# Optimization experiments

Hardware: AMD Instinct MI355X
Metric: run time of the kernel (lower is better)

The kernel has to match this reference:

```python
import jax, jax.numpy as jnp
import numpy as np

SEP = 2            # sep_token_id
B, S, H = 8, 4096, 768
MAX_SENT = 64      # = labels.size(1) in the original
STD = 0.02         # initializer_range


def setup_inputs() -> dict:
    key = jax.random.key(0)
    ks = jax.random.split(key, 6)
    hidden = jax.random.normal(ks[0], (B, S, H), jnp.float32)
    ids = jax.random.randint(ks[1], (B, S), 5, 30000, dtype=jnp.int64)
    # plant a sep every 64 tokens -> 64 seps, 64 non-empty sentences per row
    ids = ids.at[:, 63::64].set(SEP)
    W1 = jax.random.normal(ks[2], (H, 4096), jnp.float32) * STD
    b1 = jnp.zeros((4096,), jnp.float32)
    W2 = jax.random.normal(ks[3], (4096, 256), jnp.float32) * STD
    b2 = jnp.zeros((256,), jnp.float32)
    W3 = jax.random.normal(ks[4], (256, 2), jnp.float32) * STD
    b3 = jnp.zeros((2,), jnp.float32)
    return dict(hidden=hidden, input_ids=ids, W1=W1, b1=b1, W2=W2, b2=b2, W3=W3, b3=b3)


def _pool_row(h, ids):
    # h: [S, H], ids: [S] -> per-sentence means [MAX_SENT, H]
    sep = (ids == SEP)
    sep_i = sep.astype(jnp.int32)
    # exclusive cumsum: segment id = number of seps strictly before position t
    seg = jnp.cumsum(sep_i) - sep_i
    pos = jnp.arange(S)
    first_sep = jnp.argmax(sep)
    n_sep = sep_i.sum()
    # original includes the FIRST sep in sentence 0 but excludes later seps,
    # and excludes the last token of the trailing (post-last-sep) segment
    weight = jnp.where(sep, pos == first_sep, True)
    weight = weight & ~((pos == S - 1) & (seg == n_sep) & (n_sep > 0))
    # truncate to max_sentences: overflow segments land in a dump bucket
    seg_c = jnp.minimum(seg, MAX_SENT)
    hw = jnp.where(weight[:, None], h, 0.0)
    sums = jax.ops.segment_sum(hw, seg_c, num_segments=MAX_SENT + 1)[:MAX_SENT]
    cnts = jax.ops.segment_sum(weight.astype(h.dtype), seg_c, num_segments=MAX_SENT + 1)[:MAX_SENT]
    # empty (padding) segments -> zeros, matching the original zero-padding
    return jnp.where(cnts[:, None] > 0, sums / jnp.maximum(cnts, 1.0)[:, None], 0.0)


def reference(hidden, input_ids, W1, b1, W2, b2, W3, b3):
    # [B, MAX_SENT, H] per-sentence mean representations
    sent = jax.vmap(_pool_row)(hidden, input_ids)
    # classifier head (dropout = identity in eval); GELU is exact (torch nn.GELU default)
    x = jax.nn.gelu(jnp.einsum('bmh,hf->bmf', sent, W1) + b1, approximate=False)
    x = jax.nn.gelu(jnp.einsum('bmf,fg->bmg', x, W2) + b2, approximate=False)
    logits = jnp.einsum('bmg,gc->bmc', x, W3) + b3  # [B, MAX_SENT, 2]
    return logits
```

## Files before the change

### kernel.cpp

```cpp
#include <hip/hip_runtime.h>
#include <hip/hip_bf16.h>

#define SEP_ID 2
#define S_LEN  4096
#define HID    768
#define MAXS   64

using short8  = __attribute__((ext_vector_type(8))) short;
using floatx4 = __attribute__((ext_vector_type(4))) float;

__device__ __forceinline__ float gelu_exact(float x) {
    return 0.5f * x * (1.0f + erff(x * 0.70710678118654752f));
}

__global__ __launch_bounds__(256) void stage1_kernel(const int* __restrict__ ids,
                                                     const float* __restrict__ hidden,
                                                     const float* __restrict__ W1,
                                                     const float* __restrict__ W2,
                                                     __hip_bfloat16* __restrict__ W1T,
                                                     __hip_bfloat16* __restrict__ W2T,
                                                     __hip_bfloat16* __restrict__ sentb) {
    __shared__ __align__(16) char smem[16640];
    const int blk = blockIdx.x;
    const int t = threadIdx.x;

    if (blk < 512) {
        int* sep_pos = (int*)smem;
        int* wtot    = sep_pos + 4096;
        const int sidx = blk;
        const int b = sidx >> 6, m = sidx & 63;
        const int* row = ids + (size_t)b * S_LEN;
        const int lane = t & 63, w = t >> 6;

        int local[16]; int c = 0;
        const int base = t * 16;
        #pragma unroll
        for (int q = 0; q < 4; ++q) {
            int4 v = ((const int4*)row)[t * 4 + q];
            if (v.x == SEP_ID) local[c++] = base + q * 4 + 0;
            if (v.y == SEP_ID) local[c++] = base + q * 4 + 1;
            if (v.z == SEP_ID) local[c++] = base + q * 4 + 2;
            if (v.w == SEP_ID) local[c++] = base + q * 4 + 3;
        }
        int scan = c;
        #pragma unroll
        for (int off = 1; off < 64; off <<= 1) {
            int n = __shfl_up(scan, off);
            if (lane >= off) scan += n;
        }
        if (lane == 63) wtot[w] = scan;
        __syncthreads();
        int wbase = 0;
        for (int i = 0; i < w; ++i) wbase += wtot[i];
        const int o = wbase + scan - c;
        for (int i = 0; i < c; ++i) sep_pos[o + i] = local[i];
        __syncthreads();
        const int n_sep = wtot[0] + wtot[1] + wtot[2] + wtot[3];

        int start = 0, cnt = 0;
        if (n_sep == 0) {
            if (m == 0) { start = 0; cnt = S_LEN; }
        } else if (m < n_sep) {
            if (m == 0) { start = 0; cnt = sep_pos[0] + 1; }
            else { start = sep_pos[m - 1] + 1; cnt = sep_pos[m] - sep_pos[m - 1] - 1; }
        } else if (m == n_sep) {
            start = sep_pos[n_sep - 1] + 1;
            cnt = (S_LEN - 1) - start;
            if (cnt < 0) cnt = 0;
        }

        if (t < 192) {
            const float4* bp = (const float4*)(hidden + ((size_t)b * S_LEN + start) * HID);
            float ax = 0.f, ay = 0.f, az = 0.f, aw = 0.f;
            int i = 0;
            for (; i + 8 <= cnt; i += 8) {
                float4 v[8];
                #pragma unroll
                for (int j = 0; j < 8; ++j) v[j] = bp[(size_t)(i + j) * 192 + t];
                #pragma unroll
                for (int j = 0; j < 8; ++j) { ax += v[j].x; ay += v[j].y; az += v[j].z; aw += v[j].w; }
            }
            for (; i < cnt; ++i) {
                float4 v = bp[(size_t)i * 192 + t];
                ax += v.x; ay += v.y; az += v.z; aw += v.w;
            }
            const float inv = (cnt > 0) ? 1.0f / (float)cnt : 0.0f;
            __hip_bfloat16* o2 = sentb + (size_t)sidx * HID + t * 4;
            o2[0] = __float2bfloat16(ax * inv);
            o2[1] = __float2bfloat16(ay * inv);
            o2[2] = __float2bfloat16(az * inv);
            o2[3] = __float2bfloat16(aw * inv);
        }
    } else {
        float* tile = (float*)smem;
        const int id0 = blk - 512;
        const float* in; __hip_bfloat16* outw; int K, N, n0, k0;
        if (id0 < 3072) { in = W1; outw = W1T; K = 768;  N = 4096;
                          n0 = (id0 & 127) * 32; k0 = (id0 >> 7) * 32; }
        else { const int id = id0 - 3072;
               in = W2; outw = W2T; K = 4096; N = 256;
               n0 = (id & 7) * 32; k0 = (id >> 3) * 32; }
        const int c = t & 31;
        const int r = t >> 5;
        #pragma unroll
        for (int i = 0; i < 32; i += 8)
            tile[(r + i) * 33 + c] = in[(size_t)(k0 + r + i) * N + n0 + c];
        __syncthreads();
        #pragma unroll
        for (int i = 0; i < 32; i += 8)
            outw[(size_t)(n0 + r + i) * K + k0 + c] = __float2bfloat16(tile[c * 33 + r + i]);
    }
}

__global__ __launch_bounds__(256) void gemm1_kernel(const __hip_bfloat16* __restrict__ A,
                                                    const __hip_bfloat16* __restrict__ BT,
                                                    const float* __restrict__ bias,
                                                    __hip_bfloat16* __restrict__ out) {
    const int n0 = blockIdx.x * 64;
    const int m0 = blockIdx.y * 64;
    const int t = threadIdx.x;
    const int w = t >> 6, l = t & 63;
    const int wm = (w >> 1) * 32;
    const int wn = (w & 1) * 32;

    __shared__ __hip_bfloat16 Al[64][72];
    __shared__ __hip_bfloat16 Bl[64][72];

    floatx4 acc[2][2] = {};

    const int r  = t >> 2;
    const int ch = (t & 3) * 16;
    const __hip_bfloat16* Ag = A  + (size_t)(m0 + r) * 768 + ch;
    const __hip_bfloat16* Bg = BT + (size_t)(n0 + r) * 768 + ch;

    const int lr = l & 15;
    const int kq = (l >> 4) * 8;

    for (int k0 = 0; k0 < 768; k0 += 64) {
        short8 av0 = *(const short8*)(Ag + k0);
        short8 av1 = *(const short8*)(Ag + k0 + 8);
        short8 bv0 = *(const short8*)(Bg + k0);
        short8 bv1 = *(const short8*)(Bg + k0 + 8);
        __syncthreads();
        *(short8*)(&Al[r][ch])     = av0;
        *(short8*)(&Al[r][ch + 8]) = av1;
        *(short8*)(&Bl[r][ch])     = bv0;
        *(short8*)(&Bl[r][ch + 8]) = bv1;
        __syncthreads();

        #pragma unroll
        for (int ks = 0; ks < 64; ks += 32) {
            short8 a0 = *(const short8*)(&Al[wm + lr][ks + kq]);
            short8 a1 = *(const short8*)(&Al[wm + 16 + lr][ks + kq]);
            short8 b0 = *(const short8*)(&Bl[wn + lr][ks + kq]);
            short8 b1 = *(const short8*)(&Bl[wn + 16 + lr][ks + kq]);
            acc[0][0] = __builtin_amdgcn_mfma_f32_16x16x32_bf16(a0, b0, acc[0][0], 0, 0, 0);
            acc[0][1] = __builtin_amdgcn_mfma_f32_16x16x32_bf16(a0, b1, acc[0][1], 0, 0, 0);
            acc[1][0] = __builtin_amdgcn_mfma_f32_16x16x32_bf16(a1, b0, acc[1][0], 0, 0, 0);
            acc[1][1] = __builtin_amdgcn_mfma_f32_16x16x32_bf16(a1, b1, acc[1][1], 0, 0, 0);
        }
    }

    #pragma unroll
    for (int i = 0; i < 2; ++i) {
        #pragma unroll
        for (int j = 0; j < 2; ++j) {
            const int col  = n0 + wn + j * 16 + lr;
            const int rowb = m0 + wm + i * 16 + (l >> 4) * 4;
            const float bv = bias[col];
            #pragma unroll
            for (int rg = 0; rg < 4; ++rg) {
                float x = acc[i][j][rg] + bv;
                out[(size_t)(rowb + rg) * 4096 + col] = __float2bfloat16(gelu_exact(x));
            }
        }
    }
}

__global__ __launch_bounds__(256) void gemm2_kernel(const __hip_bfloat16* __restrict__ A,
                                                    const __hip_bfloat16* __restrict__ BT,
                                                    float* __restrict__ part) {
    const int n0 = blockIdx.x * 64;
    const int m0 = blockIdx.y * 64;
    const int s  = blockIdx.z;
    const int kb = s * 256;
    const int t = threadIdx.x;
    const int w = t >> 6, l = t & 63;
    const int wm = (w >> 1) * 32;
    const int wn = (w & 1) * 32;

    __shared__ __hip_bfloat16 Al[64][72];
    __shared__ __hip_bfloat16 Bl[64][72];

    floatx4 acc[2][2] = {};

    const int r  = t >> 2;
    const int ch = (t & 3) * 16;
    const __hip_bfloat16* Ag = A  + (size_t)(m0 + r) * 4096 + kb + ch;
    const __hip_bfloat16* Bg = BT + (size_t)(n0 + r) * 4096 + kb + ch;

    const int lr = l & 15;
    const int kq = (l >> 4) * 8;

    for (int k0 = 0; k0 < 256; k0 += 64) {
        short8 av0 = *(const short8*)(Ag + k0);
        short8 av1 = *(const short8*)(Ag + k0 + 8);
        short8 bv0 = *(const short8*)(Bg + k0);
        short8 bv1 = *(const short8*)(Bg + k0 + 8);
        __syncthreads();
        *(short8*)(&Al[r][ch])     = av0;
        *(short8*)(&Al[r][ch + 8]) = av1;
        *(short8*)(&Bl[r][ch])     = bv0;
        *(short8*)(&Bl[r][ch + 8]) = bv1;
        __syncthreads();

        #pragma unroll
        for (int ks = 0; ks < 64; ks += 32) {
            short8 a0 = *(const short8*)(&Al[wm + lr][ks + kq]);
            short8 a1 = *(const short8*)(&Al[wm + 16 + lr][ks + kq]);
            short8 b0 = *(const short8*)(&Bl[wn + lr][ks + kq]);
            short8 b1 = *(const short8*)(&Bl[wn + 16 + lr][ks + kq]);
            acc[0][0] = __builtin_amdgcn_mfma_f32_16x16x32_bf16(a0, b0, acc[0][0], 0, 0, 0);
            acc[0][1] = __builtin_amdgcn_mfma_f32_16x16x32_bf16(a0, b1, acc[0][1], 0, 0, 0);
            acc[1][0] = __builtin_amdgcn_mfma_f32_16x16x32_bf16(a1, b0, acc[1][0], 0, 0, 0);
            acc[1][1] = __builtin_amdgcn_mfma_f32_16x16x32_bf16(a1, b1, acc[1][1], 0, 0, 0);
        }
    }

    float* po = part + (size_t)s * 512 * 256;
    #pragma unroll
    for (int i = 0; i < 2; ++i) {
        #pragma unroll
        for (int j = 0; j < 2; ++j) {
            const int col  = n0 + wn + j * 16 + lr;
            const int rowb = m0 + wm + i * 16 + (l >> 4) * 4;
            #pragma unroll
            for (int rg = 0; rg < 4; ++rg)
                po[(size_t)(rowb + rg) * 256 + col] = acc[i][j][rg];
        }
    }
}

__global__ __launch_bounds__(256) void rh_kernel(const float* __restrict__ part,
                                                 const float* __restrict__ b2,
                                                 const float* __restrict__ W3,
                                                 const float* __restrict__ b3,
                                                 float* __restrict__ out) {
    const int row = blockIdx.x;
    const int c = threadIdx.x;
    const int w = c >> 6, l = c & 63;

    float s = 0.f;
    #pragma unroll
    for (int k = 0; k < 16; ++k)
        s += part[((size_t)k * 512 + row) * 256 + c];
    const float x = gelu_exact(s + b2[c]);
    float y0 = x * W3[c * 2 + 0];
    float y1 = x * W3[c * 2 + 1];
    #pragma unroll
    for (int off = 32; off; off >>= 1) {
        y0 += __shfl_down(y0, off);
        y1 += __shfl_down(y1, off);
    }
    __shared__ float r0[4], r1[4];
    if (l == 0) { r0[w] = y0; r1[w] = y1; }
    __syncthreads();
    if (c == 0) out[row * 2 + 0] = r0[0] + r0[1] + r0[2] + r0[3] + b3[0];
    if (c == 1) out[row * 2 + 1] = r1[0] + r1[1] + r1[2] + r1[3] + b3[1];
}

extern "C" void kernel_launch(void* const* d_in, const int* in_sizes, int n_in,
                              void* d_out, int out_size, void* d_ws, size_t ws_size,
                              hipStream_t stream) {
    const float* hidden = (const float*)d_in[0];
    const int*   ids    = (const int*)d_in[1];
    const float* W1     = (const float*)d_in[2];
    const float* b1     = (const float*)d_in[3];
    const float* W2     = (const float*)d_in[4];
    const float* b2     = (const float*)d_in[5];
    const float* W3     = (const float*)d_in[6];
    const float* b3     = (const float*)d_in[7];
    float* out = (float*)d_out;

    char* ws = (char*)d_ws;
    __hip_bfloat16* sentb  = (__hip_bfloat16*)(ws + 0);
    __hip_bfloat16* W1T    = (__hip_bfloat16*)(ws + 786432);
    __hip_bfloat16* W2T    = (__hip_bfloat16*)(ws + 7077888);
    __hip_bfloat16* x1     = (__hip_bfloat16*)(ws + 9175040);
    float* part            = (float*)(ws + 13369344);

    stage1_kernel<<<4608, 256, 0, stream>>>(ids, hidden, W1, W2, W1T, W2T, sentb);
    gemm1_kernel<<<dim3(64, 8), 256, 0, stream>>>(sentb, W1T, b1, x1);
    gemm2_kernel<<<dim3(4, 8, 16), 256, 0, stream>>>(x1, W2T, part);
    rh_kernel<<<512, 256, 0, stream>>>(part, b2, W3, b3, out);
}
```

Measured before the change: 195.4 us.

## Double GEMM k-tile depth, halve split-K, stage epilogue through LDS

Both GEMMs now load 128-wide k-tiles instead of 64-wide, halving the number of barrier pairs per k-loop. GEMM2's split-K drops from 16 to 8 slices, so the reduction kernel reads fewer partial buffers. GEMM1's epilogue writes GELU results to shared memory and then stores coalesced 16-byte rows, and the pooled sentence output is written as one packed 8-byte store. The cost is more LDS per block and only 256 blocks for GEMM2, which lowers parallelism on a device with many CUs.

```diff
diff --git a/kernel.cpp b/kernel.cpp
--- a/kernel.cpp
+++ b/kernel.cpp
@@ -85,11 +85,14 @@
                 ax += v.x; ay += v.y; az += v.z; aw += v.w;
             }
             const float inv = (cnt > 0) ? 1.0f / (float)cnt : 0.0f;
-            __hip_bfloat16* o2 = sentb + (size_t)sidx * HID + t * 4;
-            o2[0] = __float2bfloat16(ax * inv);
-            o2[1] = __float2bfloat16(ay * inv);
-            o2[2] = __float2bfloat16(az * inv);
-            o2[3] = __float2bfloat16(aw * inv);
+            __hip_bfloat16 h0 = __float2bfloat16(ax * inv);
+            __hip_bfloat16 h1 = __float2bfloat16(ay * inv);
+            __hip_bfloat16 h2 = __float2bfloat16(az * inv);
+            __hip_bfloat16 h3 = __float2bfloat16(aw * inv);
+            ushort4 pk;
+            pk.x = *(unsigned short*)&h0; pk.y = *(unsigned short*)&h1;
+            pk.z = *(unsigned short*)&h2; pk.w = *(unsigned short*)&h3;
+            *(ushort4*)(sentb + (size_t)sidx * HID + t * 4) = pk;
         }
     } else {
         float* tile = (float*)smem;
@@ -123,33 +126,36 @@
     const int wm = (w >> 1) * 32;
     const int wn = (w & 1) * 32;
 
-    __shared__ __hip_bfloat16 Al[64][72];
-    __shared__ __hip_bfloat16 Bl[64][72];
+    __shared__ __hip_bfloat16 Al[64][136];
+    __shared__ __hip_bfloat16 Bl[64][136];
 
     floatx4 acc[2][2] = {};
 
     const int r  = t >> 2;
-    const int ch = (t & 3) * 16;
+    const int ch = (t & 3) * 32;
     const __hip_bfloat16* Ag = A  + (size_t)(m0 + r) * 768 + ch;
     const __hip_bfloat16* Bg = BT + (size_t)(n0 + r) * 768 + ch;
 
     const int lr = l & 15;
     const int kq = (l >> 4) * 8;
 
-    for (int k0 = 0; k0 < 768; k0 += 64) {
-        short8 av0 = *(const short8*)(Ag + k0);
-        short8 av1 = *(const short8*)(Ag + k0 + 8);
-        short8 bv0 = *(const short8*)(Bg + k0);
-        short8 bv1 = *(const short8*)(Bg + k0 + 8);
-        __syncthreads();
-        *(short8*)(&Al[r][ch])     = av0;
-        *(short8*)(&Al[r][ch + 8]) = av1;
-        *(short8*)(&Bl[r][ch])     = bv0;
-        *(short8*)(&Bl[r][ch + 8]) = bv1;
-        __syncthreads();
-
-        #pragma unroll
-        for (int ks = 0; ks < 64; ks += 32) {
+    for (int k0 = 0; k0 < 768; k0 += 128) {
+        short8 av[4], bv[4];
+        #pragma unroll
+        for (int q = 0; q < 4; ++q) {
+            av[q] = *(const short8*)(Ag + k0 + q * 8);
+            bv[q] = *(const short8*)(Bg + k0 + q * 8);
+        }
+        __syncthreads();
+        #pragma unroll
+        for (int q = 0; q < 4; ++q) {
+            *(short8*)(&Al[r][ch + q * 8]) = av[q];
+            *(short8*)(&Bl[r][ch + q * 8]) = bv[q];
+        }
+        __syncthreads();
+
+        #pragma unroll
+        for (int ks = 0; ks < 128; ks += 32) {
             short8 a0 = *(const short8*)(&Al[wm + lr][ks + kq]);
             short8 a1 = *(const short8*)(&Al[wm + 16 + lr][ks + kq]);
             short8 b0 = *(const short8*)(&Bl[wn + lr][ks + kq]);
@@ -161,19 +167,31 @@
         }
     }
 
+    __syncthreads();
+    __hip_bfloat16* E = &Al[0][0];
     #pragma unroll
     for (int i = 0; i < 2; ++i) {
         #pragma unroll
         for (int j = 0; j < 2; ++j) {
-            const int col  = n0 + wn + j * 16 + lr;
-            const int rowb = m0 + wm + i * 16 + (l >> 4) * 4;
-            const float bv = bias[col];
+            const int cl = wn + j * 16 + lr;
+            const float bv = bias[n0 + cl];
             #pragma unroll
             for (int rg = 0; rg < 4; ++rg) {
+                const int rl = wm + i * 16 + (l >> 4) * 4 + rg;
                 float x = acc[i][j][rg] + bv;
-                out[(size_t)(rowb + rg) * 4096 + col] = __float2bfloat16(gelu_exact(x));
+                E[rl * 72 + cl] = __float2bfloat16(gelu_exact(x));
             }
         }
+    }
+    __syncthreads();
+    {
+        const int rr  = t >> 2;
+        const int seg = (t & 3) * 16;
+        short8 v0 = *(const short8*)(&E[rr * 72 + seg]);
+        short8 v1 = *(const short8*)(&E[rr * 72 + seg + 8]);
+        __hip_bfloat16* op = out + (size_t)(m0 + rr) * 4096 + n0 + seg;
+        *(short8*)(op)     = v0;
+        *(short8*)(op + 8) = v1;
     }
 }
 
@@ -183,39 +201,42 @@
     const int n0 = blockIdx.x * 64;
     const int m0 = blockIdx.y * 64;
     const int s  = blockIdx.z;
-    const int kb = s * 256;
+    const int kb = s * 512;
     const int t = threadIdx.x;
     const int w = t >> 6, l = t & 63;
     const int wm = (w >> 1) * 32;
     const int wn = (w & 1) * 32;
 
-    __shared__ __hip_bfloat16 Al[64][72];
-    __shared__ __hip_bfloat16 Bl[64][72];
+    __shared__ __hip_bfloat16 Al[64][136];
+    __shared__ __hip_bfloat16 Bl[64][136];
 
     floatx4 acc[2][2] = {};
 
     const int r  = t >> 2;
-    const int ch = (t & 3) * 16;
+    const int ch = (t & 3) * 32;
     const __hip_bfloat16* Ag = A  + (size_t)(m0 + r) * 4096 + kb + ch;
     const __hip_bfloat16* Bg = BT + (size_t)(n0 + r) * 4096 + kb + ch;
 
     const int lr = l & 15;
     const int kq = (l >> 4) * 8;
 
-    for (int k0 = 0; k0 < 256; k0 += 64) {
-        short8 av0 = *(const short8*)(Ag + k0);
-        short8 av1 = *(const short8*)(Ag + k0 + 8);
-        short8 bv0 = *(const short8*)(Bg + k0);
-        short8 bv1 = *(const short8*)(Bg + k0 + 8);
-        __syncthreads();
-        *(short8*)(&Al[r][ch])     = av0;
-        *(short8*)(&Al[r][ch + 8]) = av1;
-        *(short8*)(&Bl[r][ch])     = bv0;
-        *(short8*)(&Bl[r][ch + 8]) = bv1;
-        __syncthreads();
-
-        #pragma unroll
-        for (int ks = 0; ks < 64; ks += 32) {
+    for (int k0 = 0; k0 < 512; k0 += 128) {
+        short8 av[4], bv[4];
+        #pragma unroll
+        for (int q = 0; q < 4; ++q) {
+            av[q] = *(const short8*)(Ag + k0 + q * 8);
+            bv[q] = *(const short8*)(Bg + k0 + q * 8);
+        }
+        __syncthreads();
+        #pragma unroll
+        for (int q = 0; q < 4; ++q) {
+            *(short8*)(&Al[r][ch + q * 8]) = av[q];
+            *(short8*)(&Bl[r][ch + q * 8]) = bv[q];
+        }
+        __syncthreads();
+
+        #pragma unroll
+        for (int ks = 0; ks < 128; ks += 32) {
             short8 a0 = *(const short8*)(&Al[wm + lr][ks + kq]);
             short8 a1 = *(const short8*)(&Al[wm + 16 + lr][ks + kq]);
             short8 b0 = *(const short8*)(&Bl[wn + lr][ks + kq]);
@@ -252,7 +273,7 @@
 
     float s = 0.f;
     #pragma unroll
-    for (int k = 0; k < 16; ++k)
+    for (int k = 0; k < 8; ++k)
         s += part[((size_t)k * 512 + row) * 256 + c];
     const float x = gelu_exact(s + b2[c]);
     float y0 = x * W3[c * 2 + 0];
@@ -291,6 +312,6 @@
 
     stage1_kernel<<<4608, 256, 0, stream>>>(ids, hidden, W1, W2, W1T, W2T, sentb);
     gemm1_kernel<<<dim3(64, 8), 256, 0, stream>>>(sentb, W1T, b1, x1);
-    gemm2_kernel<<<dim3(4, 8, 16), 256, 0, stream>>>(x1, W2T, part);
+    gemm2_kernel<<<dim3(4, 8, 8), 256, 0, stream>>>(x1, W2T, part);
     rh_kernel<<<512, 256, 0, stream>>>(part, b2, W3, b3, out);
 }
```

Measured after the change: 195.1 us. No clear change (-0.1%).
